# Optimization experiments

Hardware: AMD Instinct MI355X
Metric: run time of the kernel (lower is better)

Reference implementation:

```python
import jax, jax.numpy as jnp
import numpy as np

B, S, D_MODEL, D_POL = 2048, 64, 768, 64
SCALE = 1.0 / np.sqrt(D_POL).astype(np.float32)  # 1/sqrt(policy_d) = 0.125


def mish(x):
    return x * jnp.tanh(jax.nn.softplus(x))


def setup_inputs() -> dict:
    key = jax.random.key(0)
    ks = jax.random.split(key, 10)
    s = lambda fan: 1.0 / np.sqrt(fan)
    return {
        "x": jax.random.normal(ks[0], (B, S, D_MODEL), dtype=jnp.float32),
        "W1": jax.random.normal(ks[1], (D_MODEL, D_MODEL), dtype=jnp.float32) * s(D_MODEL),
        "b1": jax.random.normal(ks[2], (D_MODEL,), dtype=jnp.float32) * 0.01,
        "Wq": jax.random.normal(ks[3], (D_MODEL, D_POL), dtype=jnp.float32) * s(D_MODEL),
        "bq": jax.random.normal(ks[4], (D_POL,), dtype=jnp.float32) * 0.01,
        "Wk": jax.random.normal(ks[5], (D_MODEL, D_POL), dtype=jnp.float32) * s(D_MODEL),
        "bk": jax.random.normal(ks[6], (D_POL,), dtype=jnp.float32) * 0.01,
        "Wp": jax.random.normal(ks[7], (D_POL, 4), dtype=jnp.float32) * s(D_POL),
        "bp": jax.random.normal(ks[8], (4,), dtype=jnp.float32) * 0.01,
        "indices": jax.random.randint(ks[9], (1858,), 0, 4288, dtype=jnp.int64 if jax.config.read("jax_enable_x64") else jnp.int32),
    }


def reference(x, W1, b1, Wq, bq, Wk, bk, Wp, bp, indices):
    b = x.shape[0]
    h = mish(x @ W1 + b1)                      # [B,64,768] dense1 + mish
    q = h @ Wq + bq                            # [B,64,64]
    k = h @ Wk + bk                            # [B,64,64]
    scores = jnp.einsum("bqd,bkd->bqk", q, k) * SCALE  # [B,64,64]
    # promotion head on 8th-rank keys: Linear(D_POL -> 4)
    prom = k[:, 56:64, :] @ Wp + bp            # [B,8,4]
    # transpose/split[3,1]/add/transpose == add 4th channel to first 3
    prom = prom[:, :, :3] + prom[:, :, 3:4]    # [B,8,3]
    prom = prom.reshape(b, 1, 24)
    s2 = scores[:, 48:56, 56:64].reshape(b, 64, 1)
    s2 = jnp.concatenate([s2, s2, s2], axis=-1).reshape(b, 8, 24)
    promotion = (s2 + prom).reshape(b, 3, 64)  # [B,3,64]
    policy = jnp.concatenate([scores, promotion], axis=1).reshape(b, 4288)
    return policy[:, indices]                  # [B,1858]
```

## Files before the change

### kernel.cpp

```cpp
#include <hip/hip_runtime.h>

typedef __attribute__((ext_vector_type(8))) short short8;
typedef __attribute__((ext_vector_type(4))) float f32x4;
typedef __attribute__((ext_vector_type(4))) short short4v;

#define DM 768
#define DP 64

__device__ __forceinline__ unsigned short f2bf(float f) {
  unsigned u = __float_as_uint(f);
  u = u + 0x7fffu + ((u >> 16) & 1u);
  return (unsigned short)(u >> 16);
}
__device__ __forceinline__ float bf2f(unsigned short s) {
  return __uint_as_float(((unsigned)s) << 16);
}
__device__ __forceinline__ float mishf(float v) {
  float t = __expf(fminf(v, 30.0f));
  float num = t * (t + 2.0f);
  return v * (num / (num + 2.0f));
}

__global__ void cvt_frag(const float* __restrict__ src, unsigned short* __restrict__ dst,
                         int N, int ntPer) {
  constexpr int MAXC = 192;
  constexpr int TS = MAXC + 8;
  __shared__ unsigned short tile[32 * TS];
  const int kt = blockIdx.x;
  const int nt0 = blockIdx.y * ntPer;
  const int cols = ntPer * 16;
  for (int e = threadIdx.x; e < 32 * cols; e += blockDim.x) {
    int row = e / cols, col = e - row * cols;
    tile[row * TS + col] = f2bf(src[(kt * 32 + row) * N + nt0 * 16 + col]);
  }
  __syncthreads();
  const int NT = N / 16;
  for (int s = threadIdx.x; s < ntPer * 64; s += blockDim.x) {
    int ntl = s >> 6, l = s & 63;
    int m16 = l & 15, quad = l >> 4;
    short8 v;
    #pragma unroll
    for (int j = 0; j < 8; ++j)
      v[j] = (short)tile[(quad * 8 + j) * TS + ntl * 16 + m16];
    *(short8*)(dst + ((size_t)((kt * NT + nt0 + ntl) * 64 + l)) * 8) = v;
  }
}

__global__ __launch_bounds__(1024, 4) void fused_policy(
    const float* __restrict__ x, const float* __restrict__ b1,
    const float* __restrict__ bq, const float* __restrict__ bk,
    const float* __restrict__ Wp, const float* __restrict__ bp,
    const int* __restrict__ idxs, int n_idx,
    const unsigned short* __restrict__ W1f,
    const unsigned short* __restrict__ Wqf,
    const unsigned short* __restrict__ Wkf,
    float* __restrict__ out) {
  constexpr int XS  = 136;
  constexpr int HSS = 776;
  constexpr int QKS = 72;

  __shared__ __align__(16) unsigned char smemA[64 * HSS * 2];
  __shared__ __align__(16) unsigned short qkbuf[4][64 * QKS];
  __shared__ float promf[32];

  unsigned short* hs  = (unsigned short*)smemA;
  unsigned short* xs0 = (unsigned short*)smemA;
  unsigned short* xs1 = xs0 + 64 * XS;
  float* sc = (float*)smemA;
  unsigned short* qsh = qkbuf[0];
  unsigned short* qsl = qkbuf[1];
  unsigned short* ksh = qkbuf[2];
  unsigned short* ksl = qkbuf[3];

  const int b    = blockIdx.x;
  const int tid  = threadIdx.x;
  const int wave = tid >> 6;
  const int lane = tid & 63;
  const int m16  = lane & 15;
  const int quad = lane >> 4;

  const float* xb = x + (size_t)b * (64 * DM);

  f32x4 acc[4][3];
  #pragma unroll
  for (int rt = 0; rt < 4; ++rt)
    #pragma unroll
    for (int ct = 0; ct < 3; ++ct)
      #pragma unroll
      for (int r = 0; r < 4; ++r) acc[rt][ct][r] = 0.0f;

  float b1v[3];
  #pragma unroll
  for (int ct = 0; ct < 3; ++ct) b1v[ct] = b1[wave * 48 + ct * 16 + m16];

  const unsigned short* wb = W1f + ((size_t)(wave * 3) * 64 + lane) * 8;
  short8 bcur[3], bnxt[3];
  #pragma unroll
  for (int ct = 0; ct < 3; ++ct) bcur[ct] = *(const short8*)(wb + ct * 512);

  float4 pv0, pv1;
  {
    int e0 = tid, e1 = tid + 1024;
    pv0 = *(const float4*)(xb + (e0 >> 5) * DM + (e0 & 31) * 4);
    pv1 = *(const float4*)(xb + (e1 >> 5) * DM + (e1 & 31) * 4);
  }

  for (int c = 0; c < 6; ++c) {
    unsigned short* xw = (c & 1) ? xs1 : xs0;
    {
      int e0 = tid, e1 = tid + 1024;
      short4v s4;
      s4.x = (short)f2bf(pv0.x); s4.y = (short)f2bf(pv0.y);
      s4.z = (short)f2bf(pv0.z); s4.w = (short)f2bf(pv0.w);
      *(short4v*)(xw + (e0 >> 5) * XS + (e0 & 31) * 4) = s4;
      s4.x = (short)f2bf(pv1.x); s4.y = (short)f2bf(pv1.y);
      s4.z = (short)f2bf(pv1.z); s4.w = (short)f2bf(pv1.w);
      *(short4v*)(xw + (e1 >> 5) * XS + (e1 & 31) * 4) = s4;
    }
    __syncthreads();
    if (c < 5) {
      int kb = (c + 1) * 128;
      int e0 = tid, e1 = tid + 1024;
      pv0 = *(const float4*)(xb + (e0 >> 5) * DM + kb + (e0 & 31) * 4);
      pv1 = *(const float4*)(xb + (e1 >> 5) * DM + kb + (e1 & 31) * 4);
    }
    #pragma unroll
    for (int ks = 0; ks < 4; ++ks) {
      const int kt = c * 4 + ks;
      short8 af[4];
      #pragma unroll
      for (int rt = 0; rt < 4; ++rt)
        af[rt] = *(const short8*)(xw + (rt * 16 + m16) * XS + ks * 32 + quad * 8);
      if (kt < 23) {
        #pragma unroll
        for (int ct = 0; ct < 3; ++ct)
          bnxt[ct] = *(const short8*)(wb + (kt + 1) * 24576 + ct * 512);
      }
      #pragma unroll
      for (int rt = 0; rt < 4; ++rt)
        #pragma unroll
        for (int ct = 0; ct < 3; ++ct)
          acc[rt][ct] = __builtin_amdgcn_mfma_f32_16x16x32_bf16(af[rt], bcur[ct], acc[rt][ct], 0, 0, 0);
      if (kt < 23) {
        #pragma unroll
        for (int ct = 0; ct < 3; ++ct) bcur[ct] = bnxt[ct];
      }
    }
  }
  __syncthreads();

  #pragma unroll
  for (int rt = 0; rt < 4; ++rt)
    #pragma unroll
    for (int ct = 0; ct < 3; ++ct)
      #pragma unroll
      for (int r = 0; r < 4; ++r) {
        int row = rt * 16 + quad * 4 + r;
        int col = wave * 48 + ct * 16 + m16;
        hs[row * HSS + col] = f2bf(mishf(acc[rt][ct][r] + b1v[ct]));
      }
  __syncthreads();

  {
    const int grp = wave >> 3;
    const int w8 = wave & 7;
    const int rt = w8 & 3;
    const int ch = w8 >> 2;
    const unsigned short* Wf = grp ? Wkf : Wqf;
    const float* bias = grp ? bk : bq;
    unsigned short* oh = grp ? ksh : qsh;
    unsigned short* ol = grp ? ksl : qsl;

    f32x4 acc2[2];
    #pragma unroll
    for (int ct2 = 0; ct2 < 2; ++ct2)
      #pragma unroll
      for (int r = 0; r < 4; ++r) acc2[ct2][r] = 0.0f;

    const unsigned short* wfb = Wf + ((size_t)(ch * 2) * 64 + lane) * 8;
    short8 c2[2], n2[2];
    #pragma unroll
    for (int ct2 = 0; ct2 < 2; ++ct2) c2[ct2] = *(const short8*)(wfb + ct2 * 512);

    const int arow = (rt * 16 + m16) * HSS;
    short8 a = *(const short8*)(hs + arow + quad * 8);
    for (int kt = 0; kt < 24; ++kt) {
      short8 an;
      if (kt < 23) {
        an = *(const short8*)(hs + arow + (kt + 1) * 32 + quad * 8);
        #pragma unroll
        for (int ct2 = 0; ct2 < 2; ++ct2)
          n2[ct2] = *(const short8*)(wfb + (kt + 1) * 2048 + ct2 * 512);
      }
      #pragma unroll
      for (int ct2 = 0; ct2 < 2; ++ct2)
        acc2[ct2] = __builtin_amdgcn_mfma_f32_16x16x32_bf16(a, c2[ct2], acc2[ct2], 0, 0, 0);
      if (kt < 23) {
        a = an;
        #pragma unroll
        for (int ct2 = 0; ct2 < 2; ++ct2) c2[ct2] = n2[ct2];
      }
    }
    #pragma unroll
    for (int ct2 = 0; ct2 < 2; ++ct2)
      #pragma unroll
      for (int r = 0; r < 4; ++r) {
        int row = rt * 16 + quad * 4 + r;
        int col = ch * 32 + ct2 * 16 + m16;
        float v = acc2[ct2][r] + bias[col];
        unsigned short vh = f2bf(v);
        unsigned short vl = f2bf(v - bf2f(vh));
        oh[row * QKS + col] = vh;
        ol[row * QKS + col] = vl;
      }
  }
  __syncthreads();

  {
    const int rt = wave >> 2, ctt = wave & 3;
    f32x4 a3;
    #pragma unroll
    for (int r = 0; r < 4; ++r) a3[r] = 0.0f;
    #pragma unroll
    for (int kt = 0; kt < 2; ++kt) {
      const int k0 = kt * 32;
      short8 ah = *(const short8*)(qsh + (rt * 16 + m16) * QKS + k0 + quad * 8);
      short8 al = *(const short8*)(qsl + (rt * 16 + m16) * QKS + k0 + quad * 8);
      short8 bh = *(const short8*)(ksh + (ctt * 16 + m16) * QKS + k0 + quad * 8);
      short8 bl = *(const short8*)(ksl + (ctt * 16 + m16) * QKS + k0 + quad * 8);
      a3 = __builtin_amdgcn_mfma_f32_16x16x32_bf16(ah, bh, a3, 0, 0, 0);
      a3 = __builtin_amdgcn_mfma_f32_16x16x32_bf16(ah, bl, a3, 0, 0, 0);
      a3 = __builtin_amdgcn_mfma_f32_16x16x32_bf16(al, bh, a3, 0, 0, 0);
    }
    #pragma unroll
    for (int r = 0; r < 4; ++r)
      sc[(rt * 16 + quad * 4 + r) * 64 + ctt * 16 + m16] = a3[r] * 0.125f;

    if (wave == 15 && lane < 32) {
      const int rr = lane >> 2;
      const int c = lane & 3;
      float s = bp[c];
      const int krow = (56 + rr) * QKS;
      #pragma unroll
      for (int d = 0; d < 64; ++d) {
        float kv = bf2f(ksh[krow + d]) + bf2f(ksl[krow + d]);
        s += kv * Wp[d * 4 + c];
      }
      promf[lane] = s;
    }
  }
  __syncthreads();

  float* outb = out + (size_t)b * n_idx;
  for (int i = tid; i < n_idx; i += 1024) {
    int idx = idxs[i];
    float v;
    if (idx < 4096) {
      v = sc[idx];
    } else {
      int f = idx - 4096;
      int r = f / 24;
      int j = f - r * 24;
      int jj = j / 3;
      int cc = j - jj * 3;
      v = sc[(48 + r) * 64 + 56 + jj] + promf[jj * 4 + cc] + promf[jj * 4 + 3];
    }
    outb[i] = v;
  }
}

extern "C" void kernel_launch(void* const* d_in, const int* in_sizes, int n_in,
                              void* d_out, int out_size, void* d_ws, size_t ws_size,
                              hipStream_t stream) {
  const float* x  = (const float*)d_in[0];
  const float* W1 = (const float*)d_in[1];
  const float* b1 = (const float*)d_in[2];
  const float* Wq = (const float*)d_in[3];
  const float* bq = (const float*)d_in[4];
  const float* Wk = (const float*)d_in[5];
  const float* bk = (const float*)d_in[6];
  const float* Wp = (const float*)d_in[7];
  const float* bp = (const float*)d_in[8];
  const int* idxs = (const int*)d_in[9];

  const int B = in_sizes[0] / (64 * DM);
  const int n_idx = in_sizes[9];

  unsigned short* W1f = (unsigned short*)d_ws;
  unsigned short* Wqf = W1f + 768 * 768;
  unsigned short* Wkf = Wqf + 64 * 768;

  cvt_frag<<<dim3(24, 4), 256, 0, stream>>>(W1, W1f, 768, 12);
  cvt_frag<<<dim3(24, 1), 256, 0, stream>>>(Wq, Wqf, 64, 4);
  cvt_frag<<<dim3(24, 1), 256, 0, stream>>>(Wk, Wkf, 64, 4);

  fused_policy<<<B, 1024, 0, stream>>>(x, b1, bq, bk, Wp, bp, idxs, n_idx,
                                       W1f, Wqf, Wkf, (float*)d_out);
}
```

Baseline: 771.8 us.

## Split dense1 into two column halves to shrink LDS for higher occupancy

Dense1 is now computed in two passes of 384 output columns each, and each half feeds the Q/K projection as a partial K-reduction. This shrinks the hidden-state LDS buffer so more blocks can share a CU, and the launch bound asks for higher occupancy. In exchange, the x tile is streamed from global memory twice per block and the register prefetch of W1 fragments is dropped. The tighter launch bound also risks register pressure or spills.

```diff
diff --git a/kernel.cpp b/kernel.cpp
--- a/kernel.cpp
+++ b/kernel.cpp
@@ -46,7 +46,7 @@
   }
 }
 
-__global__ __launch_bounds__(1024, 4) void fused_policy(
+__global__ __launch_bounds__(1024, 8) void fused_policy(
     const float* __restrict__ x, const float* __restrict__ b1,
     const float* __restrict__ bq, const float* __restrict__ bk,
     const float* __restrict__ Wp, const float* __restrict__ bp,
@@ -55,22 +55,22 @@
     const unsigned short* __restrict__ Wqf,
     const unsigned short* __restrict__ Wkf,
     float* __restrict__ out) {
-  constexpr int XS  = 136;
-  constexpr int HSS = 776;
-  constexpr int QKS = 72;
-
-  __shared__ __align__(16) unsigned char smemA[64 * HSS * 2];
-  __shared__ __align__(16) unsigned short qkbuf[4][64 * QKS];
+  constexpr int XS   = 104;
+  constexpr int HSH  = 392;
+  constexpr int QKS  = 72;
+
+  __shared__ __align__(16) unsigned char smemX[2 * 64 * XS * 2];
+  __shared__ __align__(16) unsigned char smemH[64 * HSH * 2];
   __shared__ float promf[32];
 
-  unsigned short* hs  = (unsigned short*)smemA;
-  unsigned short* xs0 = (unsigned short*)smemA;
+  unsigned short* xs0 = (unsigned short*)smemX;
   unsigned short* xs1 = xs0 + 64 * XS;
-  float* sc = (float*)smemA;
-  unsigned short* qsh = qkbuf[0];
-  unsigned short* qsl = qkbuf[1];
-  unsigned short* ksh = qkbuf[2];
-  unsigned short* ksl = qkbuf[3];
+  float* sc = (float*)smemX;
+  unsigned short* hsh = (unsigned short*)smemH;
+  unsigned short* qsh = hsh;
+  unsigned short* qsl = hsh + 4608;
+  unsigned short* ksh = hsh + 9216;
+  unsigned short* ksl = hsh + 13824;
 
   const int b    = blockIdx.x;
   const int tid  = threadIdx.x;
@@ -81,133 +81,112 @@
 
   const float* xb = x + (size_t)b * (64 * DM);
 
-  f32x4 acc[4][3];
+  const int rt = wave & 3;
+  const int cg = wave >> 2;
+  const int qk  = wave >> 3;
+  const int w8  = wave & 7;
+  const int rt2 = w8 & 3;
+  const int ch  = w8 >> 2;
+
+  f32x4 acc2[2];
   #pragma unroll
-  for (int rt = 0; rt < 4; ++rt)
-    #pragma unroll
-    for (int ct = 0; ct < 3; ++ct)
-      #pragma unroll
-      for (int r = 0; r < 4; ++r) acc[rt][ct][r] = 0.0f;
-
-  float b1v[3];
-  #pragma unroll
-  for (int ct = 0; ct < 3; ++ct) b1v[ct] = b1[wave * 48 + ct * 16 + m16];
-
-  const unsigned short* wb = W1f + ((size_t)(wave * 3) * 64 + lane) * 8;
-  short8 bcur[3], bnxt[3];
-  #pragma unroll
-  for (int ct = 0; ct < 3; ++ct) bcur[ct] = *(const short8*)(wb + ct * 512);
-
-  float4 pv0, pv1;
-  {
-    int e0 = tid, e1 = tid + 1024;
-    pv0 = *(const float4*)(xb + (e0 >> 5) * DM + (e0 & 31) * 4);
-    pv1 = *(const float4*)(xb + (e1 >> 5) * DM + (e1 & 31) * 4);
-  }
-
-  for (int c = 0; c < 6; ++c) {
-    unsigned short* xw = (c & 1) ? xs1 : xs0;
+  for (int c2 = 0; c2 < 2; ++c2)
+    #pragma unroll
+    for (int r = 0; r < 4; ++r) acc2[c2][r] = 0.0f;
+
+  for (int p = 0; p < 2; ++p) {
+    f32x4 acc[6];
+    #pragma unroll
+    for (int ct = 0; ct < 6; ++ct)
+      #pragma unroll
+      for (int r = 0; r < 4; ++r) acc[ct][r] = 0.0f;
+
+    const unsigned short* wb = W1f + ((size_t)((p * 24 + cg * 6) * 64) + lane) * 8;
+
+    float4 pv0, pv1;
     {
-      int e0 = tid, e1 = tid + 1024;
-      short4v s4;
-      s4.x = (short)f2bf(pv0.x); s4.y = (short)f2bf(pv0.y);
-      s4.z = (short)f2bf(pv0.z); s4.w = (short)f2bf(pv0.w);
-      *(short4v*)(xw + (e0 >> 5) * XS + (e0 & 31) * 4) = s4;
-      s4.x = (short)f2bf(pv1.x); s4.y = (short)f2bf(pv1.y);
-      s4.z = (short)f2bf(pv1.z); s4.w = (short)f2bf(pv1.w);
-      *(short4v*)(xw + (e1 >> 5) * XS + (e1 & 31) * 4) = s4;
-    }
-    __syncthreads();
-    if (c < 5) {
-      int kb = (c + 1) * 128;
-      int e0 = tid, e1 = tid + 1024;
-      pv0 = *(const float4*)(xb + (e0 >> 5) * DM + kb + (e0 & 31) * 4);
-      pv1 = *(const float4*)(xb + (e1 >> 5) * DM + kb + (e1 & 31) * 4);
-    }
-    #pragma unroll
-    for (int ks = 0; ks < 4; ++ks) {
-      const int kt = c * 4 + ks;
-      short8 af[4];
-      #pragma unroll
-      for (int rt = 0; rt < 4; ++rt)
-        af[rt] = *(const short8*)(xw + (rt * 16 + m16) * XS + ks * 32 + quad * 8);
-      if (kt < 23) {
+      int e1 = tid + 1024;
+      pv0 = *(const float4*)(xb + (tid / 24) * DM + (tid % 24) * 4);
+      if (e1 < 1536) pv1 = *(const float4*)(xb + (e1 / 24) * DM + (e1 % 24) * 4);
+    }
+
+    for (int c = 0; c < 8; ++c) {
+      unsigned short* xw = (c & 1) ? xs1 : xs0;
+      {
+        int e1 = tid + 1024;
+        short4v s4;
+        s4.x = (short)f2bf(pv0.x); s4.y = (short)f2bf(pv0.y);
+        s4.z = (short)f2bf(pv0.z); s4.w = (short)f2bf(pv0.w);
+        *(short4v*)(xw + (tid / 24) * XS + (tid % 24) * 4) = s4;
+        if (e1 < 1536) {
+          s4.x = (short)f2bf(pv1.x); s4.y = (short)f2bf(pv1.y);
+          s4.z = (short)f2bf(pv1.z); s4.w = (short)f2bf(pv1.w);
+          *(short4v*)(xw + (e1 / 24) * XS + (e1 % 24) * 4) = s4;
+        }
+      }
+      __syncthreads();
+      if (c < 7) {
+        int kb = (c + 1) * 96;
+        int e1 = tid + 1024;
+        pv0 = *(const float4*)(xb + (tid / 24) * DM + kb + (tid % 24) * 4);
+        if (e1 < 1536) pv1 = *(const float4*)(xb + (e1 / 24) * DM + kb + (e1 % 24) * 4);
+      }
+      #pragma unroll
+      for (int kk = 0; kk < 3; ++kk) {
+        const int kt = c * 3 + kk;
+        short8 af = *(const short8*)(xw + (rt * 16 + m16) * XS + kk * 32 + quad * 8);
         #pragma unroll
-        for (int ct = 0; ct < 3; ++ct)
-          bnxt[ct] = *(const short8*)(wb + (kt + 1) * 24576 + ct * 512);
-      }
-      #pragma unroll
-      for (int rt = 0; rt < 4; ++rt)
-        #pragma unroll
-        for (int ct = 0; ct < 3; ++ct)
-          acc[rt][ct] = __builtin_amdgcn_mfma_f32_16x16x32_bf16(af[rt], bcur[ct], acc[rt][ct], 0, 0, 0);
-      if (kt < 23) {
-        #pragma unroll
-        for (int ct = 0; ct < 3; ++ct) bcur[ct] = bnxt[ct];
-      }
-    }
-  }
-  __syncthreads();
-
-  #pragma unroll
-  for (int rt = 0; rt < 4; ++rt)
-    #pragma unroll
-    for (int ct = 0; ct < 3; ++ct)
+        for (int g = 0; g < 2; ++g) {
+          short8 bf[3];
+          #pragma unroll
+          for (int j = 0; j < 3; ++j)
+            bf[j] = *(const short8*)(wb + (size_t)kt * 24576 + (g * 3 + j) * 512);
+          #pragma unroll
+          for (int j = 0; j < 3; ++j)
+            acc[g * 3 + j] = __builtin_amdgcn_mfma_f32_16x16x32_bf16(af, bf[j], acc[g * 3 + j], 0, 0, 0);
+        }
+      }
+      __syncthreads();
+    }
+
+    #pragma unroll
+    for (int ct = 0; ct < 6; ++ct)
       #pragma unroll
       for (int r = 0; r < 4; ++r) {
         int row = rt * 16 + quad * 4 + r;
-        int col = wave * 48 + ct * 16 + m16;
-        hs[row * HSS + col] = f2bf(mishf(acc[rt][ct][r] + b1v[ct]));
-      }
-  __syncthreads();
+        int col = cg * 96 + ct * 16 + m16;
+        hsh[row * HSH + col] = f2bf(mishf(acc[ct][r] + b1[p * 384 + col]));
+      }
+    __syncthreads();
+
+    {
+      const unsigned short* Wf = qk ? Wkf : Wqf;
+      const unsigned short* wfb = Wf + ((size_t)((p * 12 * 4 + ch * 2) * 64) + lane) * 8;
+      const int arow = (rt2 * 16 + m16) * HSH;
+      #pragma unroll
+      for (int kt = 0; kt < 12; ++kt) {
+        short8 a = *(const short8*)(hsh + arow + kt * 32 + quad * 8);
+        #pragma unroll
+        for (int c2 = 0; c2 < 2; ++c2) {
+          short8 bf = *(const short8*)(wfb + (size_t)(kt * 4 + c2) * 512);
+          acc2[c2] = __builtin_amdgcn_mfma_f32_16x16x32_bf16(a, bf, acc2[c2], 0, 0, 0);
+        }
+      }
+    }
+    __syncthreads();
+  }
 
   {
-    const int grp = wave >> 3;
-    const int w8 = wave & 7;
-    const int rt = w8 & 3;
-    const int ch = w8 >> 2;
-    const unsigned short* Wf = grp ? Wkf : Wqf;
-    const float* bias = grp ? bk : bq;
-    unsigned short* oh = grp ? ksh : qsh;
-    unsigned short* ol = grp ? ksl : qsl;
-
-    f32x4 acc2[2];
-    #pragma unroll
-    for (int ct2 = 0; ct2 < 2; ++ct2)
-      #pragma unroll
-      for (int r = 0; r < 4; ++r) acc2[ct2][r] = 0.0f;
-
-    const unsigned short* wfb = Wf + ((size_t)(ch * 2) * 64 + lane) * 8;
-    short8 c2[2], n2[2];
-    #pragma unroll
-    for (int ct2 = 0; ct2 < 2; ++ct2) c2[ct2] = *(const short8*)(wfb + ct2 * 512);
-
-    const int arow = (rt * 16 + m16) * HSS;
-    short8 a = *(const short8*)(hs + arow + quad * 8);
-    for (int kt = 0; kt < 24; ++kt) {
-      short8 an;
-      if (kt < 23) {
-        an = *(const short8*)(hs + arow + (kt + 1) * 32 + quad * 8);
-        #pragma unroll
-        for (int ct2 = 0; ct2 < 2; ++ct2)
-          n2[ct2] = *(const short8*)(wfb + (kt + 1) * 2048 + ct2 * 512);
-      }
-      #pragma unroll
-      for (int ct2 = 0; ct2 < 2; ++ct2)
-        acc2[ct2] = __builtin_amdgcn_mfma_f32_16x16x32_bf16(a, c2[ct2], acc2[ct2], 0, 0, 0);
-      if (kt < 23) {
-        a = an;
-        #pragma unroll
-        for (int ct2 = 0; ct2 < 2; ++ct2) c2[ct2] = n2[ct2];
-      }
-    }
-    #pragma unroll
-    for (int ct2 = 0; ct2 < 2; ++ct2)
+    const float* bias = qk ? bk : bq;
+    unsigned short* oh = qk ? ksh : qsh;
+    unsigned short* ol = qk ? ksl : qsl;
+    #pragma unroll
+    for (int c2 = 0; c2 < 2; ++c2)
       #pragma unroll
       for (int r = 0; r < 4; ++r) {
-        int row = rt * 16 + quad * 4 + r;
-        int col = ch * 32 + ct2 * 16 + m16;
-        float v = acc2[ct2][r] + bias[col];
+        int row = rt2 * 16 + quad * 4 + r;
+        int col = ch * 32 + c2 * 16 + m16;
+        float v = acc2[c2][r] + bias[col];
         unsigned short vh = f2bf(v);
         unsigned short vl = f2bf(v - bf2f(vh));
         oh[row * QKS + col] = vh;
@@ -217,15 +196,15 @@
   __syncthreads();
 
   {
-    const int rt = wave >> 2, ctt = wave & 3;
+    const int rt3 = wave >> 2, ctt = wave & 3;
     f32x4 a3;
     #pragma unroll
     for (int r = 0; r < 4; ++r) a3[r] = 0.0f;
     #pragma unroll
     for (int kt = 0; kt < 2; ++kt) {
       const int k0 = kt * 32;
-      short8 ah = *(const short8*)(qsh + (rt * 16 + m16) * QKS + k0 + quad * 8);
-      short8 al = *(const short8*)(qsl + (rt * 16 + m16) * QKS + k0 + quad * 8);
+      short8 ah = *(const short8*)(qsh + (rt3 * 16 + m16) * QKS + k0 + quad * 8);
+      short8 al = *(const short8*)(qsl + (rt3 * 16 + m16) * QKS + k0 + quad * 8);
       short8 bh = *(const short8*)(ksh + (ctt * 16 + m16) * QKS + k0 + quad * 8);
       short8 bl = *(const short8*)(ksl + (ctt * 16 + m16) * QKS + k0 + quad * 8);
       a3 = __builtin_amdgcn_mfma_f32_16x16x32_bf16(ah, bh, a3, 0, 0, 0);
@@ -234,7 +213,7 @@
     }
     #pragma unroll
     for (int r = 0; r < 4; ++r)
-      sc[(rt * 16 + quad * 4 + r) * 64 + ctt * 16 + m16] = a3[r] * 0.125f;
+      sc[(rt3 * 16 + quad * 4 + r) * 64 + ctt * 16 + m16] = a3[r] * 0.125f;
 
     if (wave == 15 && lane < 32) {
       const int rr = lane >> 2;
```

After: 997.4 us. 29.2% more time.
